# Kernel tuning notes

Hardware: AMD Instinct MI355X
Metric: run time of the kernel (lower is better)

Reference implementation:

```python
import jax, jax.numpy as jnp
import numpy as np

EPS = 1e-5

def _bn(y, gamma, beta):
    # BatchNorm1d in training mode over the flattened (B*N, C) batch dim.
    m = jnp.mean(y, axis=0)
    v = jnp.var(y, axis=0)  # biased variance, matches torch normalization
    return gamma * (y - m) * jax.lax.rsqrt(v + EPS) + beta

def _hardswish(x):
    return x * jnp.clip(x + 3.0, 0.0, 6.0) / 6.0

def setup_inputs() -> dict:
    key = jax.random.key(0)
    ks = jax.random.split(key, 8)
    B, N, C, H = 16, 784, 384, 8
    res = int(N ** 0.5)  # 28
    inner = 3 * C
    x = jax.random.normal(ks[0], (B, N, C), dtype=jnp.float32)
    Wqkv = jax.random.normal(ks[1], (inner, C), dtype=jnp.float32) * (C ** -0.5)
    g1 = jnp.ones((inner,), jnp.float32) + 0.1 * jax.random.normal(ks[2], (inner,))
    b1 = 0.1 * jax.random.normal(ks[3], (inner,))
    Wproj = jax.random.normal(ks[4], (C, C), dtype=jnp.float32) * (C ** -0.5)
    g2 = jnp.ones((C,), jnp.float32) + 0.1 * jax.random.normal(ks[5], (C,))
    b2 = 0.1 * jax.random.normal(ks[6], (C,))
    biases = 0.02 * jax.random.normal(ks[7], (H, res * res), dtype=jnp.float32)
    # idx[i,j] = |dx|*res + |dy| reproduces torch's encounter-order offset ids
    coords = np.stack(np.meshgrid(np.arange(res), np.arange(res), indexing='ij'), -1).reshape(N, 2)
    d = np.abs(coords[:, None, :] - coords[None, :, :])
    bias_idxs = jnp.asarray(d[..., 0] * res + d[..., 1], dtype=jnp.int32)  # [N,N]
    return {"x": x, "Wqkv": Wqkv, "g1": g1, "b1": b1, "Wproj": Wproj,
            "g2": g2, "b2": b2, "biases": biases, "bias_idxs": bias_idxs}

def reference(x, Wqkv, g1, b1, Wproj, g2, b2, biases, bias_idxs):
    B, N, C = x.shape
    H = biases.shape[0]
    hd = C // H
    scale = hd ** -0.5
    # qkv = LinearNorm(dim, 3*dim)
    y = _bn(x.reshape(B * N, C) @ Wqkv.T, g1, b1)              # [B*N, 3C]
    qkv = y.reshape(B, N, 3, H, hd).transpose(2, 0, 3, 1, 4)   # [3,B,H,N,hd]
    q, k, v = qkv[0], qkv[1], qkv[2]
    attn = jnp.einsum('bhnd,bhmd->bhnm', q, k) * scale         # [B,H,N,N]
    attn = attn + biases[:, bias_idxs][None]                   # gathered rel-pos bias
    attn = jax.nn.softmax(attn, axis=-1)
    o = jnp.einsum('bhnm,bhmd->bhnd', attn, v)                 # [B,H,N,hd]
    o = o.transpose(0, 2, 1, 3).reshape(B, N, C)
    # proj = Hardswish -> LinearNorm(dim, dim)
    o = _hardswish(o).reshape(B * N, C)
    o = _bn(o @ Wproj.T, g2, b2)
    return o.reshape(B, N, C)
```

## Files before the change

kernel.cpp:

```cpp
#include <hip/hip_runtime.h>

#define R_TOTAL 12544
#define NTOK    784
#define CDIM    384
#define INNER   1152
#define NHEAD   8
#define HDIM    48
#define BATCH   16
#define HSEG    37632
#define SCALE   0.14433756729740643f
#define LOG2E   1.4426950408889634f
#define SCLOG2E 0.20823509f

typedef unsigned short u16;
typedef unsigned int   u32;
typedef __attribute__((ext_vector_type(8))) short short8;
typedef __attribute__((ext_vector_type(4))) float floatx4;

union V8 { uint4 u; short8 s; u16 h[8]; };

#define OB_OFF     28901376ull
#define ST_OFF     38535168ull

__device__ __forceinline__ float b2f(u16 u) {
    union { float f; u32 i; } v; v.i = ((u32)u) << 16; return v.f;
}
__device__ __forceinline__ u16 f2b(float f) {
    union { float f; u32 i; } v; v.f = f;
    u32 r = v.i + 0x7FFFu + ((v.i >> 16) & 1u);
    return (u16)(r >> 16);
}
__device__ __forceinline__ u32 pk2(float lo, float hi) {
    union { float f; u32 i; } a, b; a.f = lo; b.f = hi;
    u32 ra = a.i + 0x7FFFu + ((a.i >> 16) & 1u);
    u32 rb = b.i + 0x7FFFu + ((b.i >> 16) & 1u);
    return __builtin_amdgcn_perm(rb, ra, 0x07060302u);
}
__device__ __forceinline__ float hswish_f(float v) {
    return v * fminf(fmaxf(v + 3.f, 0.f), 6.f) * (1.f / 6.f);
}

__global__ __launch_bounds__(256) void zero_k(float* __restrict__ p, int n) {
    int i = blockIdx.x * 256 + threadIdx.x;
    if (i < n) p[i] = 0.f;
}

template<int ABF16, int HSW, int OBF16, int HEADM>
__global__ __launch_bounds__(256) void gemm_mfma_k(
    const void* __restrict__ Ap, const float* __restrict__ Bfp,
    void* __restrict__ Cp, float* __restrict__ sums, int M, int Nout, int K)
{
    __shared__ u16 As[128 * 40];
    __shared__ u16 Bs[128 * 40];
    const int t = threadIdx.x;
    const int lane = t & 63, wv = t >> 6;
    const int l15 = lane & 15, quad = lane >> 4;
    const int wm = (wv & 1) * 64, wn = (wv >> 1) * 64;
    const int m0 = blockIdx.y * 128, n0 = blockIdx.x * 128;
    const floatx4 zf = {0.f, 0.f, 0.f, 0.f};

    floatx4 acc[4][4];
    #pragma unroll
    for (int i = 0; i < 4; i++)
        #pragma unroll
        for (int j = 0; j < 4; j++) acc[i][j] = zf;

    for (int k0 = 0; k0 < K; k0 += 32) {
        __syncthreads();
        #pragma unroll
        for (int it = 0; it < 2; it++) {
            const int flat = t + it * 256;
            const int rr = flat >> 2, ss = (flat & 3) * 8;
            uint4 aw;
            if (ABF16) {
                uint4 u = *(const uint4*)((const u16*)Ap + (size_t)(m0 + rr) * K + k0 + ss);
                if (HSW) {
                    aw.x = pk2(hswish_f(b2f((u16)(u.x & 0xffff))), hswish_f(b2f((u16)(u.x >> 16))));
                    aw.y = pk2(hswish_f(b2f((u16)(u.y & 0xffff))), hswish_f(b2f((u16)(u.y >> 16))));
                    aw.z = pk2(hswish_f(b2f((u16)(u.z & 0xffff))), hswish_f(b2f((u16)(u.z >> 16))));
                    aw.w = pk2(hswish_f(b2f((u16)(u.w & 0xffff))), hswish_f(b2f((u16)(u.w >> 16))));
                } else {
                    aw = u;
                }
            } else {
                const float* p = (const float*)Ap + (size_t)(m0 + rr) * K + k0 + ss;
                float4 f0 = *(const float4*)p, f1 = *(const float4*)(p + 4);
                aw.x = pk2(f0.x, f0.y); aw.y = pk2(f0.z, f0.w);
                aw.z = pk2(f1.x, f1.y); aw.w = pk2(f1.z, f1.w);
            }
            *(uint4*)&As[rr * 40 + ss] = aw;
            const float* q = Bfp + (size_t)(n0 + rr) * K + k0 + ss;
            float4 g0 = *(const float4*)q, g1 = *(const float4*)(q + 4);
            uint4 bw;
            bw.x = pk2(g0.x, g0.y); bw.y = pk2(g0.z, g0.w);
            bw.z = pk2(g1.x, g1.y); bw.w = pk2(g1.z, g1.w);
            *(uint4*)&Bs[rr * 40 + ss] = bw;
        }
        __syncthreads();
        short8 af[4], bfr[4];
        #pragma unroll
        for (int mi = 0; mi < 4; mi++)
            af[mi] = *(const short8*)&As[(wm + mi * 16 + l15) * 40 + quad * 8];
        #pragma unroll
        for (int ni = 0; ni < 4; ni++)
            bfr[ni] = *(const short8*)&Bs[(wn + ni * 16 + l15) * 40 + quad * 8];
        #pragma unroll
        for (int mi = 0; mi < 4; mi++)
            #pragma unroll
            for (int ni = 0; ni < 4; ni++)
                acc[mi][ni] = __builtin_amdgcn_mfma_f32_16x16x32_bf16(af[mi], bfr[ni], acc[mi][ni], 0, 0, 0);
    }

    float cs[4] = {0.f, 0.f, 0.f, 0.f}, cq[4] = {0.f, 0.f, 0.f, 0.f};
    #pragma unroll
    for (int mi = 0; mi < 4; mi++) {
        const int mbase = m0 + wm + mi * 16 + quad * 4;
        int bb_[4], nn_[4];
        if (HEADM) {
            #pragma unroll
            for (int reg = 0; reg < 4; reg++) {
                int m = mbase + reg;
                int bv = ((m >> 4) * 1338) >> 16;
                bb_[reg] = bv;
                nn_[reg] = m - bv * 784;
            }
        }
        #pragma unroll
        for (int ni = 0; ni < 4; ni++) {
            const int c0 = n0 + wn + ni * 16;
            const int n = c0 + l15;
            int part = 0, hcol = 0, d0 = 0;
            if (HEADM) {
                part = c0 / 384;
                int rem = c0 - part * 384;
                hcol = rem / 48;
                d0 = rem - hcol * 48;
            }
            if (HEADM && part == 2) {
                u32 w0 = pk2(acc[mi][ni][0], acc[mi][ni][1]);
                u32 w1 = pk2(acc[mi][ni][2], acc[mi][ni][3]);
                size_t off = (size_t)((bb_[0] * 8 + hcol) * 3 + 2) * HSEG
                           + (size_t)(d0 + l15) * NTOK + nn_[0];
                *(uint2*)((u16*)Cp + off) = make_uint2(w0, w1);
                float v0 = b2f((u16)(w0 & 0xffff)), v1 = b2f((u16)(w0 >> 16));
                float v2 = b2f((u16)(w1 & 0xffff)), v3 = b2f((u16)(w1 >> 16));
                cs[ni] += (v0 + v1) + (v2 + v3);
                cq[ni] += (v0 * v0 + v1 * v1) + (v2 * v2 + v3 * v3);
            } else {
                #pragma unroll
                for (int reg = 0; reg < 4; reg++) {
                    float v = acc[mi][ni][reg];
                    float vv;
                    if (OBF16) {
                        u16 hv = f2b(v);
                        size_t off;
                        if (HEADM)
                            off = (size_t)((bb_[reg] * 8 + hcol) * 3 + part) * HSEG
                                + (size_t)nn_[reg] * 48 + d0 + l15;
                        else
                            off = (size_t)(mbase + reg) * Nout + n;
                        ((u16*)Cp)[off] = hv;
                        vv = b2f(hv);
                    } else {
                        ((float*)Cp)[(size_t)(mbase + reg) * Nout + n] = v;
                        vv = v;
                    }
                    cs[ni] += vv;
                    cq[ni] += vv * vv;
                }
            }
        }
    }
    #pragma unroll
    for (int ni = 0; ni < 4; ni++) {
        float s = cs[ni], sq = cq[ni];
        s  += __shfl_xor(s, 16);  s  += __shfl_xor(s, 32);
        sq += __shfl_xor(sq, 16); sq += __shfl_xor(sq, 32);
        if (quad == 0) {
            int col = n0 + wn + ni * 16 + l15;
            atomicAdd(&sums[col], s);
            atomicAdd(&sums[Nout + col], sq);
        }
    }
}

__global__ __launch_bounds__(256) void finalize_bn_k(
    const float* __restrict__ sums, const float* __restrict__ g,
    const float* __restrict__ bvec, float* __restrict__ ab, int Ncols, float invM,
    int sc0, int sc1, float sfac)
{
    int c = blockIdx.x * 256 + threadIdx.x;
    if (c >= Ncols) return;
    float mean = sums[c] * invM;
    float var  = sums[Ncols + c] * invM - mean * mean;
    float a    = g[c] * rsqrtf(var + 1e-5f);
    float f    = (c >= sc0 && c < sc1) ? sfac : 1.f;
    ab[c] = a * f;
    ab[Ncols + c] = (bvec[c] - mean * a) * f;
}

__global__ __launch_bounds__(256) void bn_apply_k(
    float* __restrict__ Z, const float* __restrict__ ab, int Ncols, int total4)
{
    for (int i4 = blockIdx.x * 256 + threadIdx.x; i4 < total4; i4 += gridDim.x * 256) {
        int col = (i4 * 4) % Ncols;
        float4 z  = *(float4*)(Z + (size_t)i4 * 4);
        float4 a4 = *(const float4*)(ab + col);
        float4 b4 = *(const float4*)(ab + Ncols + col);
        z.x = a4.x * z.x + b4.x; z.y = a4.y * z.y + b4.y;
        z.z = a4.z * z.z + b4.z; z.w = a4.w * z.w + b4.w;
        *(float4*)(Z + (size_t)i4 * 4) = z;
    }
}

__global__ __launch_bounds__(256) void bn_apply_bf16_k(
    u16* __restrict__ Z, const float* __restrict__ ab, int total8)
{
    int i8 = blockIdx.x * 256 + threadIdx.x;
    if (i8 >= total8) return;
    int e0  = i8 * 8;
    int seg = e0 / HSEG;
    int rem = e0 - seg * HSEG;
    int part = seg % 3;
    int hh   = (seg / 3) & 7;
    uint4 u = *(uint4*)(Z + (size_t)i8 * 8);
    uint4 o;
    if (part == 2) {
        int dd  = rem / NTOK;
        int col = 2 * 384 + hh * 48 + dd;
        float a = ab[col], bb = ab[1152 + col];
        o.x = pk2(fmaf(b2f((u16)(u.x & 0xffff)), a, bb), fmaf(b2f((u16)(u.x >> 16)), a, bb));
        o.y = pk2(fmaf(b2f((u16)(u.y & 0xffff)), a, bb), fmaf(b2f((u16)(u.y >> 16)), a, bb));
        o.z = pk2(fmaf(b2f((u16)(u.z & 0xffff)), a, bb), fmaf(b2f((u16)(u.z >> 16)), a, bb));
        o.w = pk2(fmaf(b2f((u16)(u.w & 0xffff)), a, bb), fmaf(b2f((u16)(u.w >> 16)), a, bb));
    } else {
        int d0  = rem % 48;
        int col = part * 384 + hh * 48 + d0;
        float4 A0 = *(const float4*)(ab + col),        A1 = *(const float4*)(ab + col + 4);
        float4 B0 = *(const float4*)(ab + 1152 + col), B1 = *(const float4*)(ab + 1152 + col + 4);
        o.x = pk2(fmaf(b2f((u16)(u.x & 0xffff)), A0.x, B0.x), fmaf(b2f((u16)(u.x >> 16)), A0.y, B0.y));
        o.y = pk2(fmaf(b2f((u16)(u.y & 0xffff)), A0.z, B0.z), fmaf(b2f((u16)(u.y >> 16)), A0.w, B0.w));
        o.z = pk2(fmaf(b2f((u16)(u.z & 0xffff)), A1.x, B1.x), fmaf(b2f((u16)(u.z >> 16)), A1.y, B1.y));
        o.w = pk2(fmaf(b2f((u16)(u.w & 0xffff)), A1.z, B1.z), fmaf(b2f((u16)(u.w >> 16)), A1.w, B1.w));
    }
    *(uint4*)(Z + (size_t)i8 * 8) = o;
}

__global__ __launch_bounds__(256) void attn_mfma_k(
    const u16* __restrict__ Y,
    const float* __restrict__ biases, const int* __restrict__ idxs,
    u16* __restrict__ O)
{
    __shared__ u16 psm[4][2][2 * 64 * 8];
    __shared__ float hb[NTOK];

    const int t = threadIdx.x;
    const int lane = t & 63, wv = t >> 6;
    const int l15 = lane & 15, quad = lane >> 4;
    const int bh = blockIdx.x;
    const int b = bh >> 3, h = bh & 7;
    const int n0 = blockIdx.y * 128;
    const int bN = b * NTOK;
    const floatx4 zf = {0.f, 0.f, 0.f, 0.f};

    const u16* Qb = Y + (size_t)(bh * 3) * HSEG;
    const u16* Kb = Qb + HSEG;
    const u16* Vb = Qb + 2 * HSEG;

    if (t < 196) {
        float4 v = *(const float4*)(biases + (size_t)h * NTOK + (t << 2));
        v.x *= LOG2E; v.y *= LOG2E; v.z *= LOG2E; v.w *= LOG2E;
        *(float4*)&hb[t << 2] = v;
    }

    int qv[2], qr[2];
    #pragma unroll
    for (int qh = 0; qh < 2; qh++) {
        qv[qh] = n0 + qh * 64 + wv * 16 + l15;
        qr[qh] = qv[qh] < NTOK ? qv[qh] : NTOK - 1;
    }
    const int* idxrow[2] = { idxs + (size_t)qr[0] * NTOK, idxs + (size_t)qr[1] * NTOK };

    short8 qf[2][2];
    #pragma unroll
    for (int qh = 0; qh < 2; qh++) {
        V8 a0, a1;
        a1.u = make_uint4(0u, 0u, 0u, 0u);
        const u16* src = Qb + (size_t)qr[qh] * 48;
        a0.u = *(const uint4*)(src + quad * 8);
        if (quad < 2) a1.u = *(const uint4*)(src + 32 + quad * 8);
        qf[qh][0] = a0.s; qf[qh][1] = a1.s;
    }

    V8 kfr[4][2];
    #pragma unroll
    for (int sub = 0; sub < 4; sub++) {
        const u16* src = Kb + (size_t)(sub * 16 + l15) * 48;
        kfr[sub][0].u = *(const uint4*)(src + quad * 8);
        kfr[sub][1].u = *(const uint4*)(src + 32 + quad * 8);
    }

    float lsum[2] = {0.f, 0.f};
    floatx4 oacc[2][3];
    #pragma unroll
    for (int qh = 0; qh < 2; qh++)
        #pragma unroll
        for (int i = 0; i < 3; i++) oacc[qh][i] = zf;

    const int psbase = ((quad >> 1) * 16 + l15) * 8 + (quad & 1) * 4;

    __syncthreads();

    for (int mt = 0; mt < 13; mt++) {
        const int m0k = mt * 64;
        const bool tail = (m0k == 768);

        int4 ivc[2][4];
        #pragma unroll
        for (int qh = 0; qh < 2; qh++)
            #pragma unroll
            for (int sub = 0; sub < 4; sub++) {
                int kb = m0k + sub * 16 + quad * 4;
                kb = kb < NTOK - 4 ? kb : NTOK - 4;
                ivc[qh][sub] = *(const int4*)(idxrow[qh] + kb);
            }

        short8 vfr[2][3];
        #pragma unroll
        for (int kc = 0; kc < 2; kc++) {
            int kk = m0k + kc * 32 + quad * 8;
            kk = kk <= NTOK - 8 ? kk : 0;
            #pragma unroll
            for (int ns = 0; ns < 3; ns++)
                vfr[kc][ns] = *(const short8*)(Vb + (size_t)(ns * 16 + l15) * NTOK + kk);
        }

        V8 kn[4][2];
        const bool more = (mt + 1 < 13);
        if (more) {
            const int mn = m0k + 64;
            #pragma unroll
            for (int sub = 0; sub < 4; sub++) {
                int key = mn + sub * 16 + l15;
                int kr  = key < NTOK ? key : NTOK - 1;
                const u16* src = Kb + (size_t)kr * 48;
                kn[sub][0].u = *(const uint4*)(src + quad * 8);
                kn[sub][1].u = *(const uint4*)(src + 32 + quad * 8);
            }
        }

        #pragma unroll
        for (int qh = 0; qh < 2; qh++) {
            floatx4 sf[4];
            #pragma unroll
            for (int sub = 0; sub < 4; sub++) {
                floatx4 c = zf;
                c = __builtin_amdgcn_mfma_f32_16x16x32_bf16(kfr[sub][0].s, qf[qh][0], c, 0, 0, 0);
                c = __builtin_amdgcn_mfma_f32_16x16x32_bf16(kfr[sub][1].s, qf[qh][1], c, 0, 0, 0);
                sf[sub] = c;
            }
            #pragma unroll
            for (int sub = 0; sub < 4; sub++) {
                const int4 iv = ivc[qh][sub];
                float a0 = sf[sub][0] + hb[iv.x];
                float a1 = sf[sub][1] + hb[iv.y];
                float a2 = sf[sub][2] + hb[iv.z];
                float a3 = sf[sub][3] + hb[iv.w];
                float pr[4];
                asm("v_exp_f32 %0, %1" : "=v"(pr[0]) : "v"(a0));
                asm("v_exp_f32 %0, %1" : "=v"(pr[1]) : "v"(a1));
                asm("v_exp_f32 %0, %1" : "=v"(pr[2]) : "v"(a2));
                asm("v_exp_f32 %0, %1" : "=v"(pr[3]) : "v"(a3));
                if (tail) {
                    const int kb0 = m0k + sub * 16 + quad * 4;
                    #pragma unroll
                    for (int reg = 0; reg < 4; reg++)
                        if (kb0 + reg >= NTOK) pr[reg] = 0.f;
                }
                lsum[qh] += (pr[0] + pr[1]) + (pr[2] + pr[3]);
                int addr = psbase + (sub >> 1) * 512 + (sub & 1) * 256;
                *(uint2*)&psm[wv][qh][addr] = make_uint2(pk2(pr[0], pr[1]), pk2(pr[2], pr[3]));
            }
        }

        #pragma unroll
        for (int kc = 0; kc < 2; kc++) {
            short8 pb0 = *(const short8*)&psm[wv][0][(kc * 64 + lane) * 8];
            short8 pb1 = *(const short8*)&psm[wv][1][(kc * 64 + lane) * 8];
            #pragma unroll
            for (int ns = 0; ns < 3; ns++) {
                oacc[0][ns] = __builtin_amdgcn_mfma_f32_16x16x32_bf16(vfr[kc][ns], pb0, oacc[0][ns], 0, 0, 0);
                oacc[1][ns] = __builtin_amdgcn_mfma_f32_16x16x32_bf16(vfr[kc][ns], pb1, oacc[1][ns], 0, 0, 0);
            }
        }

        if (more) {
            #pragma unroll
            for (int sub = 0; sub < 4; sub++) {
                kfr[sub][0] = kn[sub][0];
                kfr[sub][1] = kn[sub][1];
            }
        }
    }

    #pragma unroll
    for (int qh = 0; qh < 2; qh++) {
        float ls = lsum[qh];
        ls += __shfl_xor(ls, 16);
        ls += __shfl_xor(ls, 32);
        if (qv[qh] < NTOK) {
            float rl = 1.f / ls;
            u16* dst = O + (size_t)(bN + qv[qh]) * CDIM + h * HDIM;
            #pragma unroll
            for (int ns = 0; ns < 3; ns++)
                #pragma unroll
                for (int reg = 0; reg < 4; reg++)
                    dst[ns * 16 + quad * 4 + reg] = f2b(hswish_f(oacc[qh][ns][reg] * rl));
        }
    }
}

extern "C" void kernel_launch(void* const* d_in, const int* in_sizes, int n_in,
                              void* d_out, int out_size, void* d_ws, size_t ws_size,
                              hipStream_t stream)
{
    const float* x     = (const float*)d_in[0];
    const float* Wqkv  = (const float*)d_in[1];
    const float* g1    = (const float*)d_in[2];
    const float* b1    = (const float*)d_in[3];
    const float* Wproj = (const float*)d_in[4];
    const float* g2    = (const float*)d_in[5];
    const float* b2    = (const float*)d_in[6];
    const float* bias  = (const float*)d_in[7];
    const int*   idxs  = (const int*)d_in[8];
    float* out = (float*)d_out;
    char*  wsb = (char*)d_ws;

    u16*   Yb  = (u16*)wsb;
    u16*   Ob  = (u16*)(wsb + OB_OFF);
    float* S1  = (float*)(wsb + ST_OFF);
    float* AB1 = S1 + 2304;
    float* S2  = AB1 + 2304;
    float* AB2 = S2 + 768;

    zero_k<<<24, 256, 0, stream>>>(S1, 6144);

    gemm_mfma_k<0, 0, 1, 1><<<dim3(INNER / 128, R_TOTAL / 128), 256, 0, stream>>>(
        x, Wqkv, Yb, S1, R_TOTAL, INNER, CDIM);

    finalize_bn_k<<<(INNER + 255) / 256, 256, 0, stream>>>(
        S1, g1, b1, AB1, INNER, 1.f / R_TOTAL, CDIM, 2 * CDIM, SCLOG2E);
    bn_apply_bf16_k<<<(R_TOTAL * INNER / 8 + 255) / 256, 256, 0, stream>>>(
        Yb, AB1, R_TOTAL * INNER / 8);

    attn_mfma_k<<<dim3(NHEAD * BATCH, 7), 256, 0, stream>>>(Yb, bias, idxs, Ob);

    gemm_mfma_k<1, 0, 0, 0><<<dim3(CDIM / 128, R_TOTAL / 128), 256, 0, stream>>>(
        Ob, Wproj, out, S2, R_TOTAL, CDIM, CDIM);

    finalize_bn_k<<<(CDIM + 255) / 256, 256, 0, stream>>>(
        S2, g2, b2, AB2, CDIM, 1.f / R_TOTAL, 0, 0, 1.f);
    bn_apply_k<<<1024, 256, 0, stream>>>(out, AB2, CDIM, (R_TOTAL * CDIM) / 4);
}
```

Measured before the change: 247.3 us.

## Shrink attention query tile to 64 rows and drop K prefetch double-buffer

The attention kernel now processes 64 queries per block instead of 128, nearly doubling the grid (13 row-blocks per batch-head) and halving per-thread accumulators and LDS. K fragments are loaded each iteration instead of being prefetched one tile ahead, and a min-blocks-per-CU hint of 5 is added to push occupancy. This aims for more parallelism and latency hiding through occupancy. In exchange, K/V and index loads are amortized over fewer queries, so global and L2 traffic rises, and the software prefetch is lost.

Result: slower. 256.0 us (+3.5%).

```diff
diff --git a/kernel.cpp b/kernel.cpp
--- a/kernel.cpp
+++ b/kernel.cpp
@@ -246,12 +246,12 @@
     *(uint4*)(Z + (size_t)i8 * 8) = o;
 }
 
-__global__ __launch_bounds__(256) void attn_mfma_k(
+__global__ __launch_bounds__(256, 5) void attn_mfma_k(
     const u16* __restrict__ Y,
     const float* __restrict__ biases, const int* __restrict__ idxs,
     u16* __restrict__ O)
 {
-    __shared__ u16 psm[4][2][2 * 64 * 8];
+    __shared__ u16 psm[4][64 * 8 * 2];
     __shared__ float hb[NTOK];
 
     const int t = threadIdx.x;
@@ -259,7 +259,7 @@
     const int l15 = lane & 15, quad = lane >> 4;
     const int bh = blockIdx.x;
     const int b = bh >> 3, h = bh & 7;
-    const int n0 = blockIdx.y * 128;
+    const int n0 = blockIdx.y * 64;
     const int bN = b * NTOK;
     const floatx4 zf = {0.f, 0.f, 0.f, 0.f};
 
@@ -273,39 +273,24 @@
         *(float4*)&hb[t << 2] = v;
     }
 
-    int qv[2], qr[2];
-    #pragma unroll
-    for (int qh = 0; qh < 2; qh++) {
-        qv[qh] = n0 + qh * 64 + wv * 16 + l15;
-        qr[qh] = qv[qh] < NTOK ? qv[qh] : NTOK - 1;
-    }
-    const int* idxrow[2] = { idxs + (size_t)qr[0] * NTOK, idxs + (size_t)qr[1] * NTOK };
-
-    short8 qf[2][2];
-    #pragma unroll
-    for (int qh = 0; qh < 2; qh++) {
+    const int qv = n0 + wv * 16 + l15;
+    const int qr = qv < NTOK ? qv : NTOK - 1;
+    const int* idxrow = idxs + (size_t)qr * NTOK;
+
+    short8 qf[2];
+    {
         V8 a0, a1;
         a1.u = make_uint4(0u, 0u, 0u, 0u);
-        const u16* src = Qb + (size_t)qr[qh] * 48;
+        const u16* src = Qb + (size_t)qr * 48;
         a0.u = *(const uint4*)(src + quad * 8);
         if (quad < 2) a1.u = *(const uint4*)(src + 32 + quad * 8);
-        qf[qh][0] = a0.s; qf[qh][1] = a1.s;
-    }
-
-    V8 kfr[4][2];
+        qf[0] = a0.s; qf[1] = a1.s;
+    }
+
+    float lsum = 0.f;
+    floatx4 oacc[3];
     #pragma unroll
-    for (int sub = 0; sub < 4; sub++) {
-        const u16* src = Kb + (size_t)(sub * 16 + l15) * 48;
-        kfr[sub][0].u = *(const uint4*)(src + quad * 8);
-        kfr[sub][1].u = *(const uint4*)(src + 32 + quad * 8);
-    }
-
-    float lsum[2] = {0.f, 0.f};
-    floatx4 oacc[2][3];
-    #pragma unroll
-    for (int qh = 0; qh < 2; qh++)
-        #pragma unroll
-        for (int i = 0; i < 3; i++) oacc[qh][i] = zf;
+    for (int i = 0; i < 3; i++) oacc[i] = zf;
 
     const int psbase = ((quad >> 1) * 16 + l15) * 8 + (quad & 1) * 4;
 
@@ -315,15 +300,23 @@
         const int m0k = mt * 64;
         const bool tail = (m0k == 768);
 
-        int4 ivc[2][4];
-        #pragma unroll
-        for (int qh = 0; qh < 2; qh++)
-            #pragma unroll
-            for (int sub = 0; sub < 4; sub++) {
-                int kb = m0k + sub * 16 + quad * 4;
-                kb = kb < NTOK - 4 ? kb : NTOK - 4;
-                ivc[qh][sub] = *(const int4*)(idxrow[qh] + kb);
-            }
+        int4 ivc[4];
+        #pragma unroll
+        for (int sub = 0; sub < 4; sub++) {
+            int kb = m0k + sub * 16 + quad * 4;
+            kb = kb < NTOK - 4 ? kb : NTOK - 4;
+            ivc[sub] = *(const int4*)(idxrow + kb);
+        }
+
+        V8 kfr[4][2];
+        #pragma unroll
+        for (int sub = 0; sub < 4; sub++) {
+            int key = m0k + sub * 16 + l15;
+            int kr  = key < NTOK ? key : NTOK - 1;
+            const u16* src = Kb + (size_t)kr * 48;
+            kfr[sub][0].u = *(const uint4*)(src + quad * 8);
+            kfr[sub][1].u = *(const uint4*)(src + 32 + quad * 8);
+        }
 
         short8 vfr[2][3];
         #pragma unroll
@@ -335,87 +328,59 @@
                 vfr[kc][ns] = *(const short8*)(Vb + (size_t)(ns * 16 + l15) * NTOK + kk);
         }
 
-        V8 kn[4][2];
-        const bool more = (mt + 1 < 13);
-        if (more) {
-            const int mn = m0k + 64;
+        floatx4 sf[4];
+        #pragma unroll
+        for (int sub = 0; sub < 4; sub++) {
+            floatx4 c = zf;
+            c = __builtin_amdgcn_mfma_f32_16x16x32_bf16(kfr[sub][0].s, qf[0], c, 0, 0, 0);
+            c = __builtin_amdgcn_mfma_f32_16x16x32_bf16(kfr[sub][1].s, qf[1], c, 0, 0, 0);
+            sf[sub] = c;
+        }
+
+        #pragma unroll
+        for (int sub = 0; sub < 4; sub++) {
+            const int4 iv = ivc[sub];
+            float a0 = sf[sub][0] + hb[iv.x];
+            float a1 = sf[sub][1] + hb[iv.y];
+            float a2 = sf[sub][2] + hb[iv.z];
+            float a3 = sf[sub][3] + hb[iv.w];
+            float pr[4];
+            asm("v_exp_f32 %0, %1" : "=v"(pr[0]) : "v"(a0));
+            asm("v_exp_f32 %0, %1" : "=v"(pr[1]) : "v"(a1));
+            asm("v_exp_f32 %0, %1" : "=v"(pr[2]) : "v"(a2));
+            asm("v_exp_f32 %0, %1" : "=v"(pr[3]) : "v"(a3));
+            if (tail) {
+                const int kb0 = m0k + sub * 16 + quad * 4;
+                #pragma unroll
+                for (int reg = 0; reg < 4; reg++)
+                    if (kb0 + reg >= NTOK) pr[reg] = 0.f;
+            }
+            lsum += (pr[0] + pr[1]) + (pr[2] + pr[3]);
+            int addr = psbase + (sub >> 1) * 512 + (sub & 1) * 256;
+            *(uint2*)&psm[wv][addr] = make_uint2(pk2(pr[0], pr[1]), pk2(pr[2], pr[3]));
+        }
+
+        #pragma unroll
+        for (int kc = 0; kc < 2; kc++) {
+            short8 pb = *(const short8*)&psm[wv][(kc * 64 + lane) * 8];
             #pragma unroll
-            for (int sub = 0; sub < 4; sub++) {
-                int key = mn + sub * 16 + l15;
-                int kr  = key < NTOK ? key : NTOK - 1;
-                const u16* src = Kb + (size_t)kr * 48;
-                kn[sub][0].u = *(const uint4*)(src + quad * 8);
-                kn[sub][1].u = *(const uint4*)(src + 32 + quad * 8);
-            }
-        }
-
-        #pragma unroll
-        for (int qh = 0; qh < 2; qh++) {
-            floatx4 sf[4];
-            #pragma unroll
-            for (int sub = 0; sub < 4; sub++) {
-                floatx4 c = zf;
-                c = __builtin_amdgcn_mfma_f32_16x16x32_bf16(kfr[sub][0].s, qf[qh][0], c, 0, 0, 0);
-                c = __builtin_amdgcn_mfma_f32_16x16x32_bf16(kfr[sub][1].s, qf[qh][1], c, 0, 0, 0);
-                sf[sub] = c;
-            }
-            #pragma unroll
-            for (int sub = 0; sub < 4; sub++) {
-                const int4 iv = ivc[qh][sub];
-                float a0 = sf[sub][0] + hb[iv.x];
-                float a1 = sf[sub][1] + hb[iv.y];
-                float a2 = sf[sub][2] + hb[iv.z];
-                float a3 = sf[sub][3] + hb[iv.w];
-                float pr[4];
-                asm("v_exp_f32 %0, %1" : "=v"(pr[0]) : "v"(a0));
-                asm("v_exp_f32 %0, %1" : "=v"(pr[1]) : "v"(a1));
-                asm("v_exp_f32 %0, %1" : "=v"(pr[2]) : "v"(a2));
-                asm("v_exp_f32 %0, %1" : "=v"(pr[3]) : "v"(a3));
-                if (tail) {
-                    const int kb0 = m0k + sub * 16 + quad * 4;
-                    #pragma unroll
-                    for (int reg = 0; reg < 4; reg++)
-                        if (kb0 + reg >= NTOK) pr[reg] = 0.f;
-                }
-                lsum[qh] += (pr[0] + pr[1]) + (pr[2] + pr[3]);
-                int addr = psbase + (sub >> 1) * 512 + (sub & 1) * 256;
-                *(uint2*)&psm[wv][qh][addr] = make_uint2(pk2(pr[0], pr[1]), pk2(pr[2], pr[3]));
-            }
-        }
-
-        #pragma unroll
-        for (int kc = 0; kc < 2; kc++) {
-            short8 pb0 = *(const short8*)&psm[wv][0][(kc * 64 + lane) * 8];
-            short8 pb1 = *(const short8*)&psm[wv][1][(kc * 64 + lane) * 8];
-            #pragma unroll
-            for (int ns = 0; ns < 3; ns++) {
-                oacc[0][ns] = __builtin_amdgcn_mfma_f32_16x16x32_bf16(vfr[kc][ns], pb0, oacc[0][ns], 0, 0, 0);
-                oacc[1][ns] = __builtin_amdgcn_mfma_f32_16x16x32_bf16(vfr[kc][ns], pb1, oacc[1][ns], 0, 0, 0);
-            }
-        }
-
-        if (more) {
-            #pragma unroll
-            for (int sub = 0; sub < 4; sub++) {
-                kfr[sub][0] = kn[sub][0];
-                kfr[sub][1] = kn[sub][1];
-            }
-        }
-    }
-
-    #pragma unroll
-    for (int qh = 0; qh < 2; qh++) {
-        float ls = lsum[qh];
+            for (int ns = 0; ns < 3; ns++)
+                oacc[ns] = __builtin_amdgcn_mfma_f32_16x16x32_bf16(vfr[kc][ns], pb, oacc[ns], 0, 0, 0);
+        }
+    }
+
+    {
+        float ls = lsum;
         ls += __shfl_xor(ls, 16);
         ls += __shfl_xor(ls, 32);
-        if (qv[qh] < NTOK) {
+        if (qv < NTOK) {
             float rl = 1.f / ls;
-            u16* dst = O + (size_t)(bN + qv[qh]) * CDIM + h * HDIM;
+            u16* dst = O + (size_t)(bN + qv) * CDIM + h * HDIM;
             #pragma unroll
             for (int ns = 0; ns < 3; ns++)
                 #pragma unroll
                 for (int reg = 0; reg < 4; reg++)
-                    dst[ns * 16 + quad * 4 + reg] = f2b(hswish_f(oacc[qh][ns][reg] * rl));
+                    dst[ns * 16 + quad * 4 + reg] = f2b(hswish_f(oacc[ns][reg] * rl));
         }
     }
 }
@@ -453,7 +418,7 @@
     bn_apply_bf16_k<<<(R_TOTAL * INNER / 8 + 255) / 256, 256, 0, stream>>>(
         Yb, AB1, R_TOTAL * INNER / 8);
 
-    attn_mfma_k<<<dim3(NHEAD * BATCH, 7), 256, 0, stream>>>(Yb, bias, idxs, Ob);
+    attn_mfma_k<<<dim3(NHEAD * BATCH, 13), 256, 0, stream>>>(Yb, bias, idxs, Ob);
 
     gemm_mfma_k<1, 0, 0, 0><<<dim3(CDIM / 128, R_TOTAL / 128), 256, 0, stream>>>(
         Ob, Wproj, out, S2, R_TOTAL, CDIM, CDIM);
```

## Pre-convert GEMM operands to bf16 and stage tiles via global_load_lds

Applied to the files above, without the earlier changes.

Adds a conversion kernel that casts x, Wqkv and Wproj to bf16 in workspace buffers before the two GEMMs. The GEMM loop then copies tiles straight into LDS with global_load_lds, so per-tile fp32 loads, packing and register staging go away. The cost is extra conversion passes and launches, aliasing of workspace and output buffers, and an unpadded LDS stride of 32 that may cause bank conflicts.

Measured after the change: 241.0 us. 2.5% less time.

```diff
diff --git a/kernel.cpp b/kernel.cpp
--- a/kernel.cpp
+++ b/kernel.cpp
@@ -40,18 +40,37 @@
     return v * fminf(fmaxf(v + 3.f, 0.f), 6.f) * (1.f / 6.f);
 }
 
+__device__ __forceinline__ void gll16(const void* g, void* l) {
+    __builtin_amdgcn_global_load_lds(
+        (const __attribute__((address_space(1))) void*)g,
+        (__attribute__((address_space(3))) void*)l, 16, 0, 0);
+}
+
 __global__ __launch_bounds__(256) void zero_k(float* __restrict__ p, int n) {
     int i = blockIdx.x * 256 + threadIdx.x;
     if (i < n) p[i] = 0.f;
 }
 
-template<int ABF16, int HSW, int OBF16, int HEADM>
-__global__ __launch_bounds__(256) void gemm_mfma_k(
-    const void* __restrict__ Ap, const float* __restrict__ Bfp,
-    void* __restrict__ Cp, float* __restrict__ sums, int M, int Nout, int K)
-{
-    __shared__ u16 As[128 * 40];
-    __shared__ u16 Bs[128 * 40];
+__global__ __launch_bounds__(256) void cvt8_k(
+    const float* __restrict__ src, u16* __restrict__ dst, int total8)
+{
+    int i = blockIdx.x * 256 + threadIdx.x;
+    if (i >= total8) return;
+    const float* p = src + (size_t)i * 8;
+    float4 f0 = *(const float4*)p, f1 = *(const float4*)(p + 4);
+    uint4 o;
+    o.x = pk2(f0.x, f0.y); o.y = pk2(f0.z, f0.w);
+    o.z = pk2(f1.x, f1.y); o.w = pk2(f1.z, f1.w);
+    *(uint4*)(dst + (size_t)i * 8) = o;
+}
+
+template<int OBF16, int HEADM>
+__global__ __launch_bounds__(256) void gemm_bb_k(
+    const u16* __restrict__ A, const u16* __restrict__ B,
+    void* __restrict__ Cp, float* __restrict__ sums, int Nout, int K)
+{
+    __shared__ u16 As[128 * 32];
+    __shared__ u16 Bs[128 * 32];
     const int t = threadIdx.x;
     const int lane = t & 63, wv = t >> 6;
     const int l15 = lane & 15, quad = lane >> 4;
@@ -71,39 +90,18 @@
         for (int it = 0; it < 2; it++) {
             const int flat = t + it * 256;
             const int rr = flat >> 2, ss = (flat & 3) * 8;
-            uint4 aw;
-            if (ABF16) {
-                uint4 u = *(const uint4*)((const u16*)Ap + (size_t)(m0 + rr) * K + k0 + ss);
-                if (HSW) {
-                    aw.x = pk2(hswish_f(b2f((u16)(u.x & 0xffff))), hswish_f(b2f((u16)(u.x >> 16))));
-                    aw.y = pk2(hswish_f(b2f((u16)(u.y & 0xffff))), hswish_f(b2f((u16)(u.y >> 16))));
-                    aw.z = pk2(hswish_f(b2f((u16)(u.z & 0xffff))), hswish_f(b2f((u16)(u.z >> 16))));
-                    aw.w = pk2(hswish_f(b2f((u16)(u.w & 0xffff))), hswish_f(b2f((u16)(u.w >> 16))));
-                } else {
-                    aw = u;
-                }
-            } else {
-                const float* p = (const float*)Ap + (size_t)(m0 + rr) * K + k0 + ss;
-                float4 f0 = *(const float4*)p, f1 = *(const float4*)(p + 4);
-                aw.x = pk2(f0.x, f0.y); aw.y = pk2(f0.z, f0.w);
-                aw.z = pk2(f1.x, f1.y); aw.w = pk2(f1.z, f1.w);
-            }
-            *(uint4*)&As[rr * 40 + ss] = aw;
-            const float* q = Bfp + (size_t)(n0 + rr) * K + k0 + ss;
-            float4 g0 = *(const float4*)q, g1 = *(const float4*)(q + 4);
-            uint4 bw;
-            bw.x = pk2(g0.x, g0.y); bw.y = pk2(g0.z, g0.w);
-            bw.z = pk2(g1.x, g1.y); bw.w = pk2(g1.z, g1.w);
-            *(uint4*)&Bs[rr * 40 + ss] = bw;
-        }
+            gll16(A + (size_t)(m0 + rr) * K + k0 + ss, As + (size_t)flat * 8);
+            gll16(B + (size_t)(n0 + rr) * K + k0 + ss, Bs + (size_t)flat * 8);
+        }
+        asm volatile("s_waitcnt vmcnt(0)" ::: "memory");
         __syncthreads();
         short8 af[4], bfr[4];
         #pragma unroll
         for (int mi = 0; mi < 4; mi++)
-            af[mi] = *(const short8*)&As[(wm + mi * 16 + l15) * 40 + quad * 8];
+            af[mi] = *(const short8*)&As[(wm + mi * 16 + l15) * 32 + quad * 8];
         #pragma unroll
         for (int ni = 0; ni < 4; ni++)
-            bfr[ni] = *(const short8*)&Bs[(wn + ni * 16 + l15) * 40 + quad * 8];
+            bfr[ni] = *(const short8*)&Bs[(wn + ni * 16 + l15) * 32 + quad * 8];
         #pragma unroll
         for (int mi = 0; mi < 4; mi++)
             #pragma unroll
@@ -443,10 +441,16 @@
     float* S2  = AB1 + 2304;
     float* AB2 = S2 + 768;
 
+    u16* xb  = (u16*)(wsb + OB_OFF);
+    u16* wqb = (u16*)d_out;
+    u16* wpb = (u16*)wsb;
+
+    cvt8_k<<<(R_TOTAL * CDIM / 8 + 255) / 256, 256, 0, stream>>>(x, xb, R_TOTAL * CDIM / 8);
+    cvt8_k<<<(INNER * CDIM / 8 + 255) / 256, 256, 0, stream>>>(Wqkv, wqb, INNER * CDIM / 8);
     zero_k<<<24, 256, 0, stream>>>(S1, 6144);
 
-    gemm_mfma_k<0, 0, 1, 1><<<dim3(INNER / 128, R_TOTAL / 128), 256, 0, stream>>>(
-        x, Wqkv, Yb, S1, R_TOTAL, INNER, CDIM);
+    gemm_bb_k<1, 1><<<dim3(INNER / 128, R_TOTAL / 128), 256, 0, stream>>>(
+        xb, wqb, Yb, S1, INNER, CDIM);
 
     finalize_bn_k<<<(INNER + 255) / 256, 256, 0, stream>>>(
         S1, g1, b1, AB1, INNER, 1.f / R_TOTAL, CDIM, 2 * CDIM, SCLOG2E);
@@ -455,8 +459,9 @@
 
     attn_mfma_k<<<dim3(NHEAD * BATCH, 7), 256, 0, stream>>>(Yb, bias, idxs, Ob);
 
-    gemm_mfma_k<1, 0, 0, 0><<<dim3(CDIM / 128, R_TOTAL / 128), 256, 0, stream>>>(
-        Ob, Wproj, out, S2, R_TOTAL, CDIM, CDIM);
+    cvt8_k<<<(CDIM * CDIM / 8 + 255) / 256, 256, 0, stream>>>(Wproj, wpb, CDIM * CDIM / 8);
+    gemm_bb_k<0, 0><<<dim3(CDIM / 128, R_TOTAL / 128), 256, 0, stream>>>(
+        Ob, wpb, out, S2, CDIM, CDIM);
 
     finalize_bn_k<<<(CDIM + 255) / 256, 256, 0, stream>>>(
         S2, g2, b2, AB2, CDIM, 1.f / R_TOTAL, 0, 0, 1.f);
```
